# Performance work log

Hardware: AMD Instinct MI355X
Metric: run time of the kernel (lower is better)

## Reference

```python
import jax, jax.numpy as jnp
import numpy as np

# (C,H,W) of x0..x11; flattened size +1 homogeneous coordinate per key
SHAPES = [(3,32,32),(96,32,32),(96,32,32),(96,16,16),(192,16,16),(192,16,16),(192,8,8),(192,8,8),(192,8,8),(640,1,1),(100,1,1),(10,1,1)]
# (Cin,Cout,k,stride,pad) for conv1..conv9
CONV = [(3,96,3,1,1),(96,96,3,1,1),(96,96,3,2,1),(96,192,3,1,1),(192,192,3,1,1),(192,192,3,2,1),(192,192,3,1,1),(192,192,1,1,0),(192,10,1,1,0)]
B = 128


def setup_inputs():
    key = jax.random.key(0)
    inp = {}
    k, key = jax.random.split(key)
    inp['x0'] = jax.random.normal(k, (int(np.prod(SHAPES[0])) + 1, B), jnp.float32)
    for i, s in enumerate(SHAPES):
        n = int(np.prod(s)) + 1
        k1, k2, key = jax.random.split(key, 3)
        inp['perm%d' % i] = jax.random.permutation(k1, n)
        inp['diag%d' % i] = jax.random.uniform(k2, (n,), jnp.float32, 0.5, 1.5)
    for j, (ci, co, ks, st, pd) in enumerate(CONV):
        k1, k2, key = jax.random.split(key, 3)
        inp['w%d' % (j + 1)] = jax.random.normal(k1, (co, ci, ks, ks), jnp.float32) / np.float32(np.sqrt(ci * ks * ks))
        inp['b%d' % (j + 1)] = jax.random.normal(k2, (co,), jnp.float32) * 0.01
    k1, k2, k3, k4 = jax.random.split(key, 4)
    inp['fw1'] = jax.random.normal(k1, (100, 640), jnp.float32) / np.float32(np.sqrt(640))
    inp['fb1'] = jax.random.normal(k2, (100,), jnp.float32) * 0.01
    inp['fw2'] = jax.random.normal(k3, (10, 100), jnp.float32) / np.float32(np.sqrt(100))
    inp['fb2'] = jax.random.normal(k4, (10,), jnp.float32) * 0.01
    return inp


def _decode(x, perm, diag):
    # A_inv @ x with A_inv = P^T D^{-1}; P^T gather index is argsort(perm)
    return (x / diag[:, None])[jnp.argsort(perm)]


def _encode(y, perm, diag):
    # A @ y with A = D P; (P y)[i] = y[perm[i]]
    return diag[:, None] * y[perm]


def _conv_aug(v, w, b, shape_in, stride, pad):
    # affine-augmented conv: [W b; 0 1] applied to [feat; t]
    C, H, Wd = shape_in
    feat, t = v[:-1], v[-1]                      # (C*H*W, B), (B,)
    x = feat.T.reshape(-1, C, H, Wd)
    y = jax.lax.conv_general_dilated(x, w, (stride, stride), [(pad, pad), (pad, pad)],
                                     dimension_numbers=('NCHW', 'OIHW', 'NCHW'))
    y = y + b[None, :, None, None] * t[:, None, None, None]
    yf = y.reshape(y.shape[0], -1).T             # (N_out, B)
    return jnp.concatenate([yf, t[None, :]], axis=0)


def _fc_aug(v, w, b):
    feat, t = v[:-1], v[-1]
    return jnp.concatenate([w @ feat + b[:, None] * t[None, :], t[None, :]], axis=0)


def _forward(x0, perms, diags, ws, bs, fw1, fb1, fw2, fb2):
    x = x0
    for i in range(9):
        v = _decode(x, perms[i], diags[i])
        y = _conv_aug(v, ws[i], bs[i], SHAPES[i], CONV[i][3], CONV[i][4])
        x = jax.nn.relu(_encode(y, perms[i + 1], diags[i + 1]))
    v = _decode(x, perms[9], diags[9])
    x = jax.nn.relu(_encode(_fc_aug(v, fw1, fb1), perms[10], diags[10]))
    v = _decode(x, perms[10], diags[10])
    return _encode(_fc_aug(v, fw2, fb2), perms[11], diags[11])


def reference(x0, perm0, perm1, perm2, perm3, perm4, perm5, perm6, perm7, perm8, perm9, perm10, perm11,
              diag0, diag1, diag2, diag3, diag4, diag5, diag6, diag7, diag8, diag9, diag10, diag11,
              w1, b1, w2, b2, w3, b3, w4, b4, w5, b5, w6, b6, w7, b7, w8, b8, w9, b9,
              fw1, fb1, fw2, fb2):
    perms = [perm0, perm1, perm2, perm3, perm4, perm5, perm6, perm7, perm8, perm9, perm10, perm11]
    diags = [diag0, diag1, diag2, diag3, diag4, diag5, diag6, diag7, diag8, diag9, diag10, diag11]
    ws = [w1, w2, w3, w4, w5, w6, w7, w8, w9]
    bs = [b1, b2, b3, b4, b5, b6, b7, b8, b9]
    return _forward(x0, perms, diags, ws, bs, fw1, fb1, fw2, fb2)
```

## Files before the change

kernel.cpp:

```cpp
#include <hip/hip_runtime.h>


#define B 128
#define ZPAD 2048

typedef _Float16 f16_t;
typedef __attribute__((ext_vector_type(8))) _Float16 f16x8;
typedef __attribute__((ext_vector_type(4))) _Float16 f16x4;
typedef __attribute__((ext_vector_type(4))) float f32x4;


__global__ void decode_kernel(const float* __restrict__ x, const int* __restrict__ perm,
                              const float* __restrict__ diag, float* __restrict__ v, int nrows) {
    int row = blockIdx.x * 8 + (threadIdx.x >> 5);
    if (row >= nrows) return;
    int lane = threadIdx.x & 31;
    int p = perm[row];
    float inv = 1.0f / diag[row];
    float4 val = ((const float4*)(x + (size_t)row * B))[lane];
    val.x *= inv; val.y *= inv; val.z *= inv; val.w *= inv;
    ((float4*)(v + (size_t)p * B))[lane] = val;
}

__global__ void fc_kernel(const float* __restrict__ v, const float* __restrict__ w,
                          const float* __restrict__ b, float* __restrict__ y,
                          int K, int R, int do_relu) {
    int r = blockIdx.x;
    int n = threadIdx.x;
    float t = v[(size_t)K * B + n];
    float val;
    if (r == R) {
        val = t;
    } else {
        float a0 = 0.f, a1 = 0.f, a2 = 0.f, a3 = 0.f;
        float a4 = 0.f, a5 = 0.f, a6 = 0.f, a7 = 0.f;
        const float* wr = w + (size_t)r * K;
        int k = 0;
        for (; k + 8 <= K; k += 8) {
            float4 w0 = *(const float4*)(wr + k);
            float4 w1 = *(const float4*)(wr + k + 4);
            float x0 = v[(size_t)(k + 0) * B + n];
            float x1 = v[(size_t)(k + 1) * B + n];
            float x2 = v[(size_t)(k + 2) * B + n];
            float x3 = v[(size_t)(k + 3) * B + n];
            float x4 = v[(size_t)(k + 4) * B + n];
            float x5 = v[(size_t)(k + 5) * B + n];
            float x6 = v[(size_t)(k + 6) * B + n];
            float x7 = v[(size_t)(k + 7) * B + n];
            a0 = fmaf(w0.x, x0, a0);
            a1 = fmaf(w0.y, x1, a1);
            a2 = fmaf(w0.z, x2, a2);
            a3 = fmaf(w0.w, x3, a3);
            a4 = fmaf(w1.x, x4, a4);
            a5 = fmaf(w1.y, x5, a5);
            a6 = fmaf(w1.z, x6, a6);
            a7 = fmaf(w1.w, x7, a7);
        }
        for (; k < K; ++k)
            a0 = fmaf(wr[k], v[(size_t)k * B + n], a0);
        val = b[r] * t + ((a0 + a1) + (a2 + a3)) + ((a4 + a5) + (a6 + a7));
    }
    if (do_relu) val = fmaxf(val, 0.f);
    y[(size_t)r * B + n] = val;
}

__global__ void fc2_encode_kernel(const float* __restrict__ v, const float* __restrict__ w,
                                  const float* __restrict__ b, const int* __restrict__ perm,
                                  const float* __restrict__ diag, float* __restrict__ out) {
    int jrow = blockIdx.x;
    int n = threadIdx.x;
    int r = perm[jrow];
    float d = diag[jrow];
    float t = v[100 * B + n];
    float val;
    if (r == 10) {
        val = t;
    } else {
        float a0 = 0.f, a1 = 0.f, a2 = 0.f, a3 = 0.f;
        const float* wr = w + (size_t)r * 100;
        for (int k = 0; k < 100; k += 4) {
            float4 w4 = *(const float4*)(wr + k);
            a0 = fmaf(w4.x, v[(size_t)(k + 0) * B + n], a0);
            a1 = fmaf(w4.y, v[(size_t)(k + 1) * B + n], a1);
            a2 = fmaf(w4.z, v[(size_t)(k + 2) * B + n], a2);
            a3 = fmaf(w4.w, v[(size_t)(k + 3) * B + n], a3);
        }
        val = b[r] * t + (a0 + a1) + (a2 + a3);
    }
    out[(size_t)jrow * B + n] = d * val;
}


__global__ void pack_input_kernel(const float* __restrict__ v, f16_t* __restrict__ xout,
                                  float* __restrict__ tout) {
    int idx = blockIdx.x * 256 + threadIdx.x;
    int p = idx >> 7, n = idx & 127;
    f16x8 o = {};
    o[0] = (f16_t)v[(size_t)(0 * 1024 + p) * B + n];
    o[1] = (f16_t)v[(size_t)(1 * 1024 + p) * B + n];
    o[2] = (f16_t)v[(size_t)(2 * 1024 + p) * B + n];
    *(f16x8*)(xout + ZPAD + (size_t)p * 1024 + n * 8) = o;
    if (idx < B) tout[idx] = v[(size_t)3072 * B + idx];
}


struct WArgs {
    const float* w[9]; const float* b[9];
    int Ci[9], Co[9], KS[9], Cp[9], NCG[9];
    int woff[10]; int boff[10];
};

__global__ void pack_weights_kernel(WArgs A, f16_t* __restrict__ wp, float* __restrict__ bp,
                                    f16_t* __restrict__ x8a, f16_t* __restrict__ x8b) {
    int idx = blockIdx.x * 256 + threadIdx.x;
    if (idx < ZPAD) { x8a[idx] = (f16_t)0.f; x8b[idx] = (f16_t)0.f; }
    if (idx < A.boff[9]) {
        int l = 0;
        while (idx >= A.boff[l + 1]) ++l;
        int co = idx - A.boff[l];
        bp[idx] = (co < A.Co[l]) ? A.b[l][co] : 0.f;
    }
    if (idx >= A.woff[9]) return;
    int l = 0;
    while (idx >= A.woff[l + 1]) ++l;
    int e = idx - A.woff[l];
    int j = e & 7;
    int t1 = e >> 3;
    int Cp = A.Cp[l];
    int co = t1 % Cp;
    int gg = t1 / Cp;
    int ncg = A.NCG[l];
    int tap = gg / ncg, cg = gg - tap * ncg;
    int ks = A.KS[l];
    int kh = tap / ks, kw = tap - kh * ks;
    int ci = cg * 8 + j;
    float val = 0.f;
    if (co < A.Co[l] && tap < ks * ks && ci < A.Ci[l])
        val = A.w[l][(((size_t)co * A.Ci[l] + ci) * ks + kh) * ks + kw];
    wp[idx] = (f16_t)val;
}


template <int KS, int NS, int NSPLIT, int CBW, bool F32OUT>
__global__ __launch_bounds__(64 * CBW) void conv_mfma_kernel(
    const f16_t* __restrict__ xin, const float* __restrict__ t_in,
    const f16_t* __restrict__ wp, const float* __restrict__ bp,
    f16_t* __restrict__ xout, float* __restrict__ t_out, float* __restrict__ f32out,
    int Hi, int Wi, int Wo_log2, int HWo,
    int stride, int pad, int NCG, int nchunk, int KGr, int Co, int Co_pad,
    int PB8, int CB)
{
    constexpr int PF = 2;
    constexpr int MS = 4;
    const int wave = threadIdx.x >> 6;
    const int lane = threadIdx.x & 63;
    const int q = lane >> 4;
    const int r = lane & 15;

    const int gb = blockIdx.x;
    const int xcd = gb & 7;
    int j = gb >> 3;
    int nh = 0, cog, p;
    if (CBW > 1) {
        cog = wave;
        p = xcd * PB8 + j;
    } else {
        if (NSPLIT == 2) { nh = j & 1; j >>= 1; }
        cog = j % CB;
        p = xcd * PB8 + j / CB;
    }
    const int co0 = cog * 64;
    const int ncol0 = nh * (NS * 16);
    const int ncol8 = ncol0 * 8;

    const int ho = p >> Wo_log2;
    const int wo = p & ((1 << Wo_log2) - 1);
    const f16_t* xdata = xin + ZPAD;

    float tv[NS];
#pragma unroll
    for (int ns = 0; ns < NS; ++ns) tv[ns] = t_in[ncol0 + ns * 16 + r];

    f32x4 acc[MS][NS];
#pragma unroll
    for (int ms = 0; ms < MS; ++ms) {
        float4 b4 = *(const float4*)(bp + co0 + ms * 16 + q * 4);
#pragma unroll
        for (int ns = 0; ns < NS; ++ns) {
            acc[ms][ns][0] = b4.x * tv[ns];
            acc[ms][ns][1] = b4.y * tv[ns];
            acc[ms][ns][2] = b4.z * tv[ns];
            acc[ms][ns][3] = b4.w * tv[ns];
        }
    }

    const int hb = ho * stride - pad, wb = wo * stride - pad;
    const int HiWi = Hi * Wi;
    const int HiWi4 = 4 * HiWi;
    const int NCGHW = NCG * HiWi;
    const int wend = wb + KS;

    int g = q, cg = q, hi = hb, wi = wb, cgHW;
    {
        while (cg >= NCG) { cg -= NCG; ++wi; if (wi == wend) { wi = wb; ++hi; } }
        cgHW = cg * HiWi;
    }

    f16x8 bf[PF][NS], af[PF][MS];

    auto advance = [&]() {
        g += 4; cg += 4; cgHW += HiWi4;
        if (NCG >= 4) {
            int c2 = cg - NCG;
            bool wrap = c2 >= 0;
            int wn = wi + 1;
            bool ww = wrap & (wn == wend);
            cg   = wrap ? c2 : cg;
            cgHW = wrap ? cgHW - NCGHW : cgHW;
            wi   = wrap ? (ww ? wb : wn) : wi;
            hi   = ww ? hi + 1 : hi;
        } else {
            while (cg >= NCG) { cg -= NCG; cgHW -= NCGHW; ++wi; if (wi == wend) { wi = wb; ++hi; } }
        }
    };
    auto loadB = [&](f16x8* b) {
        bool v = (g < KGr) & ((unsigned)hi < (unsigned)Hi) & ((unsigned)wi < (unsigned)Wi);
        int boff = (cgHW + hi * Wi + wi) << 10;
        const f16_t* bb = xdata + (v ? boff : -ZPAD) + ncol8 + r * 8;
#pragma unroll
        for (int ns = 0; ns < NS; ++ns) b[ns] = *(const f16x8*)(bb + ns * 128);
    };
    auto loadA = [&](f16x8* a, int c) {
        int ac = c < nchunk ? c : nchunk - 1;
        const f16_t* ap = wp + (((ac * 4 + q) * Co_pad) + co0 + r) * 8;
#pragma unroll
        for (int ms = 0; ms < MS; ++ms) a[ms] = *(const f16x8*)(ap + ms * 128);
    };
    auto domfma = [&](f16x8* a, f16x8* b) {
#pragma unroll
        for (int ms = 0; ms < MS; ++ms)
#pragma unroll
            for (int ns = 0; ns < NS; ++ns)
                acc[ms][ns] = __builtin_amdgcn_mfma_f32_16x16x32_f16(a[ms], b[ns], acc[ms][ns], 0, 0, 0);
    };

#pragma unroll
    for (int pf = 0; pf < PF; ++pf) { loadB(bf[pf]); loadA(af[pf], pf); advance(); }
    const int nck = ((nchunk + PF - 1) / PF) * PF;
    for (int c = 0; c < nck; c += PF) {
#pragma unroll
        for (int pf = 0; pf < PF; ++pf) {
            domfma(af[pf], bf[pf]);
            loadB(bf[pf]); loadA(af[pf], c + PF + pf); advance();
        }
    }

    if (!F32OUT) {
#pragma unroll
        for (int ms = 0; ms < MS; ++ms) {
            int cob = co0 + ms * 16 + q * 4;
            if (cob < Co) {
                int off0 = ((cob >> 3) * HWo + p) * 1024 + (cob & 7) + ncol8 + r * 8;
#pragma unroll
                for (int ns = 0; ns < NS; ++ns) {
                    f16x4 h;
                    h[0] = (f16_t)fmaxf(acc[ms][ns][0], 0.f);
                    h[1] = (f16_t)fmaxf(acc[ms][ns][1], 0.f);
                    h[2] = (f16_t)fmaxf(acc[ms][ns][2], 0.f);
                    h[3] = (f16_t)fmaxf(acc[ms][ns][3], 0.f);
                    *(f16x4*)(xout + ZPAD + off0 + ns * 128) = h;
                }
            }
        }
        if (gb == 0) {
            for (int i = threadIdx.x; i < B; i += CBW * 64)
                t_out[i] = fmaxf(t_in[i], 0.f);
        }
    } else {
#pragma unroll
        for (int ms = 0; ms < MS; ++ms)
#pragma unroll
            for (int ns = 0; ns < NS; ++ns)
#pragma unroll
                for (int e = 0; e < 4; ++e) {
                    int co = co0 + ms * 16 + q * 4 + e;
                    if (co < Co)
                        f32out[((size_t)co * HWo + p) * B + ncol0 + ns * 16 + r] =
                            fmaxf(acc[ms][ns][e], 0.f);
                }
        if (gb == 0) {
            for (int i = threadIdx.x; i < B; i += CBW * 64)
                f32out[(size_t)Co * HWo * B + i] = fmaxf(t_in[i], 0.f);
        }
    }
}


extern "C" void kernel_launch(void* const* d_in, const int* in_sizes, int n_in,
                              void* d_out, int out_size, void* d_ws, size_t ws_size,
                              hipStream_t stream) {
    const float* x0 = (const float*)d_in[0];
    const int*   perm[12];
    const float* diag[12];
    for (int i = 0; i < 12; ++i) {
        perm[i] = (const int*)d_in[1 + 2 * i];
        diag[i] = (const float*)d_in[2 + 2 * i];
    }
    const float* wts[9];
    const float* bia[9];
    for (int j = 0; j < 9; ++j) {
        wts[j] = (const float*)d_in[25 + 2 * j];
        bia[j] = (const float*)d_in[26 + 2 * j];
    }
    const float* fw1 = (const float*)d_in[43];
    const float* fb1 = (const float*)d_in[44];
    const float* fw2 = (const float*)d_in[45];
    const float* fb2 = (const float*)d_in[46];
    float* out = (float*)d_out;

    static const int CiA[9]  = {3, 96, 96, 96, 192, 192, 192, 192, 192};
    static const int CoA[9]  = {96, 96, 96, 192, 192, 192, 192, 192, 10};
    static const int KSA[9]  = {3, 3, 3, 3, 3, 3, 3, 1, 1};
    static const int CpA[9]  = {128, 128, 128, 192, 192, 192, 192, 192, 64};
    static const int NCGA[9] = {1, 12, 12, 12, 24, 24, 24, 24, 24};
    static const int KGRA[9] = {9, 108, 108, 108, 216, 216, 216, 24, 24};
    static const int NCHK[9] = {3, 27, 27, 27, 54, 54, 54, 6, 6};
    static const int HiA[9]  = {32, 32, 32, 16, 16, 16, 8, 8, 8};
    static const int WoL[9]  = {5, 5, 4, 4, 4, 3, 3, 3, 3};
    static const int HWoA[9] = {1024, 1024, 256, 256, 256, 64, 64, 64, 64};
    static const int STA[9]  = {1, 1, 2, 1, 1, 2, 1, 1, 1};
    static const int PDA[9]  = {1, 1, 1, 1, 1, 1, 1, 0, 0};
    static const int NSPL[9] = {1, 1, 1, 1, 1, 2, 2, 2, 2};

    char* wsb = (char*)d_ws;
    const size_t BUF_F32  = 1574912;
    const size_t X8_BYTES = (size_t)(ZPAD + 12 * 1024 * 1024) * 2;
    float* bufA = (float*)wsb;
    float* bufB = (float*)(wsb + BUF_F32);
    f16_t* x8a  = (f16_t*)(wsb + 2 * BUF_F32);
    f16_t* x8b  = (f16_t*)(wsb + 2 * BUF_F32 + X8_BYTES);
    f16_t* wpb  = (f16_t*)(wsb + 2 * BUF_F32 + 2 * X8_BYTES);
    const size_t WP_BYTES = 2888704;
    float* bpb  = (float*)(wsb + 2 * BUF_F32 + 2 * X8_BYTES + WP_BYTES);
    float* t0   = (float*)((char*)bpb + 8192);
    float* t1   = t0 + 256;

    WArgs WA;
    int wo = 0, bo = 0;
    for (int l = 0; l < 9; ++l) {
        WA.w[l] = wts[l]; WA.b[l] = bia[l];
        WA.Ci[l] = CiA[l]; WA.Co[l] = CoA[l]; WA.KS[l] = KSA[l];
        WA.Cp[l] = CpA[l]; WA.NCG[l] = NCGA[l];
        WA.woff[l] = wo; wo += NCHK[l] * 4 * CpA[l] * 8;
        WA.boff[l] = bo; bo += CpA[l];
    }
    WA.woff[9] = wo; WA.boff[9] = bo;
    pack_weights_kernel<<<(wo + 255) / 256, 256, 0, stream>>>(WA, wpb, bpb, x8a, x8b);

    decode_kernel<<<(3073 + 7) / 8, 256, 0, stream>>>(x0, perm[0], diag[0], bufA, 3073);
    pack_input_kernel<<<131072 / 256, 256, 0, stream>>>(bufA, x8a, t0);

    f16_t* xin = x8a; f16_t* xout = x8b;
    float* tin = t0;  float* tout = t1;
    for (int l = 0; l < 9; ++l) {
        const int PB8 = HWoA[l] / 8;
        const int CB = CpA[l] / 64;
        const f16_t* wpl = wpb + WA.woff[l];
        const float* bpl = bpb + WA.boff[l];
        if (l <= 2) {
            conv_mfma_kernel<3, 8, 1, 2, false><<<8 * PB8, 128, 0, stream>>>(
                xin, tin, wpl, bpl, xout, tout, nullptr,
                HiA[l], HiA[l], WoL[l], HWoA[l], STA[l], PDA[l],
                NCGA[l], NCHK[l], KGRA[l], CoA[l], CpA[l], PB8, CB);
        } else if (l <= 4) {
            conv_mfma_kernel<3, 8, 1, 3, false><<<8 * PB8, 192, 0, stream>>>(
                xin, tin, wpl, bpl, xout, tout, nullptr,
                HiA[l], HiA[l], WoL[l], HWoA[l], STA[l], PDA[l],
                NCGA[l], NCHK[l], KGRA[l], CoA[l], CpA[l], PB8, CB);
        } else if (l <= 6) {
            conv_mfma_kernel<3, 4, 2, 1, false><<<8 * PB8 * CB * 2, 64, 0, stream>>>(
                xin, tin, wpl, bpl, xout, tout, nullptr,
                HiA[l], HiA[l], WoL[l], HWoA[l], STA[l], PDA[l],
                NCGA[l], NCHK[l], KGRA[l], CoA[l], CpA[l], PB8, CB);
        } else if (l == 7) {
            conv_mfma_kernel<1, 4, 2, 1, false><<<8 * PB8 * CB * 2, 64, 0, stream>>>(
                xin, tin, wpl, bpl, xout, tout, nullptr,
                HiA[l], HiA[l], WoL[l], HWoA[l], STA[l], PDA[l],
                NCGA[l], NCHK[l], KGRA[l], CoA[l], CpA[l], PB8, CB);
        } else {
            conv_mfma_kernel<1, 4, 2, 1, true><<<8 * PB8 * CB * 2, 64, 0, stream>>>(
                xin, tin, wpl, bpl, nullptr, nullptr, bufA,
                HiA[l], HiA[l], WoL[l], HWoA[l], STA[l], PDA[l],
                NCGA[l], NCHK[l], KGRA[l], CoA[l], CpA[l], PB8, CB);
        }
        f16_t* xt = xin; xin = xout; xout = xt;
        float* tt = tin; tin = tout; tout = tt;
    }

    fc_kernel<<<101, B, 0, stream>>>(bufA, fw1, fb1, bufB, 640, 100, 1);
    fc2_encode_kernel<<<11, B, 0, stream>>>(bufB, fw2, fb2, perm[11], diag[11], out);
}
```

Measured before the change: 330.3 us.

## Stage conv operand tiles through double-buffered LDS shared across waves

```diff
diff --git a/kernel.cpp b/kernel.cpp
--- a/kernel.cpp
+++ b/kernel.cpp
@@ -141,8 +141,193 @@
 }
 
 
-template <int KS, int NS, int NSPLIT, int CBW, bool F32OUT>
-__global__ __launch_bounds__(64 * CBW) void conv_mfma_kernel(
+template <int KS, int NS, int NSPLIT, int CBW, int CP, bool F32OUT>
+__global__ __launch_bounds__(64 * CBW, 2) void conv_lds_kernel(
+    const f16_t* __restrict__ xin, const float* __restrict__ t_in,
+    const f16_t* __restrict__ wp, const float* __restrict__ bp,
+    f16_t* __restrict__ xout, float* __restrict__ t_out, float* __restrict__ f32out,
+    int Hi, int Wi, int Wo_log2, int HWo,
+    int stride, int pad, int NCG, int nchunk, int KGr, int Co, int PB8)
+{
+    constexpr int MS = 4;
+    constexpr int ABYTES = CP * 64;
+    constexpr int BBYTES = NS * 1024;
+    constexpr int BUFSZ  = ABYTES + BBYTES;
+    constexpr int APIECE = CP / 16;
+    constexpr int BPIECE = NS;
+    constexpr int NPIECE = APIECE + BPIECE;
+    constexpr int NPT    = ((NPIECE + CBW - 1) / CBW) * CBW;
+    constexpr int S      = NPT / CBW;
+
+    __shared__ char smem[2 * BUFSZ];
+
+    const int wave = threadIdx.x >> 6;
+    const int lane = threadIdx.x & 63;
+    const int q = lane >> 4;
+    const int r = lane & 15;
+
+    const int gb = blockIdx.x;
+    const int xcd = gb & 7;
+    int j = gb >> 3;
+    int nh = 0;
+    if (NSPLIT == 2) { nh = j & 1; j >>= 1; }
+    const int p = xcd * PB8 + j;
+    const int co0 = wave * 64;
+    const int ncol0 = nh * (NS * 16);
+    const int ncol8 = ncol0 * 8;
+
+    const int ho = p >> Wo_log2;
+    const int wo = p & ((1 << Wo_log2) - 1);
+    const f16_t* xdata = xin + ZPAD;
+
+    float tv[NS];
+#pragma unroll
+    for (int ns = 0; ns < NS; ++ns) tv[ns] = t_in[ncol0 + ns * 16 + r];
+
+    f32x4 acc[MS][NS];
+#pragma unroll
+    for (int ms = 0; ms < MS; ++ms) {
+        float4 b4 = *(const float4*)(bp + co0 + ms * 16 + q * 4);
+#pragma unroll
+        for (int ns = 0; ns < NS; ++ns) {
+            acc[ms][ns][0] = b4.x * tv[ns];
+            acc[ms][ns][1] = b4.y * tv[ns];
+            acc[ms][ns][2] = b4.z * tv[ns];
+            acc[ms][ns][3] = b4.w * tv[ns];
+        }
+    }
+
+    const int hb = ho * stride - pad, wb = wo * stride - pad;
+    const int HiWi = Hi * Wi;
+    const int HiWi4 = 4 * HiWi;
+    const int NCGHW = NCG * HiWi;
+    const int wend = wb + KS;
+
+    int g4[4], cg4[4], hi4[4], wi4[4], cgHW4[4];
+#pragma unroll
+    for (int k = 0; k < 4; ++k) {
+        g4[k] = k; cg4[k] = k; hi4[k] = hb; wi4[k] = wb;
+        while (cg4[k] >= NCG) { cg4[k] -= NCG; ++wi4[k]; if (wi4[k] == wend) { wi4[k] = wb; ++hi4[k]; } }
+        cgHW4[k] = cg4[k] * HiWi;
+    }
+    auto advance = [&]() {
+#pragma unroll
+        for (int k = 0; k < 4; ++k) {
+            g4[k] += 4; cg4[k] += 4; cgHW4[k] += HiWi4;
+            while (cg4[k] >= NCG) { cg4[k] -= NCG; cgHW4[k] -= NCGHW; ++wi4[k]; if (wi4[k] == wend) { wi4[k] = wb; ++hi4[k]; } }
+        }
+    };
+
+    auto piece_loff = [&](int idx) {
+        int pi = (idx < NPIECE) ? idx : (idx - NPIECE + APIECE);
+        if (pi < APIECE) return pi * 1024;
+        int bi = pi - APIECE;
+        int k  = (NS == 8) ? (bi >> 1) : bi;
+        int jj = (NS == 8) ? (bi & 1) : 0;
+        return ABYTES + k * (NS * 256) + jj * 1024;
+    };
+
+    f16x8 sreg[S];
+    auto ldg = [&](int cc) {
+        const f16_t* abase = wp + (size_t)cc * 4 * CP * 8;
+        const f16_t* bslab[4];
+#pragma unroll
+        for (int k = 0; k < 4; ++k) {
+            bool v = (g4[k] < KGr) & ((unsigned)hi4[k] < (unsigned)Hi) & ((unsigned)wi4[k] < (unsigned)Wi);
+            int boff = (cgHW4[k] + hi4[k] * Wi + wi4[k]) << 10;
+            bslab[k] = xdata + (v ? boff : -ZPAD) + ncol8;
+        }
+#pragma unroll
+        for (int s = 0; s < S; ++s) {
+            int idx = wave + s * CBW;
+            int pi = (idx < NPIECE) ? idx : (idx - NPIECE + APIECE);
+            const f16_t* g;
+            if (pi < APIECE) {
+                g = abase + pi * 512;
+            } else {
+                int bi = pi - APIECE;
+                int k  = (NS == 8) ? (bi >> 1) : bi;
+                int jj = (NS == 8) ? (bi & 1) : 0;
+                g = bslab[k] + jj * 512;
+            }
+            sreg[s] = *(const f16x8*)(g + lane * 8);
+        }
+    };
+    auto dsw = [&](int cc) {
+        char* base = smem + (cc & 1) * BUFSZ;
+#pragma unroll
+        for (int s = 0; s < S; ++s) {
+            int loff = piece_loff(wave + s * CBW);
+            *(f16x8*)(base + loff + lane * 16) = sreg[s];
+        }
+    };
+    auto comp = [&](int cc) {
+        const char* base = smem + (cc & 1) * BUFSZ;
+        f16x8 af[MS], bf[NS];
+#pragma unroll
+        for (int ms = 0; ms < MS; ++ms)
+            af[ms] = *(const f16x8*)(base + ((q * CP) + co0 + ms * 16 + r) * 16);
+#pragma unroll
+        for (int ns = 0; ns < NS; ++ns)
+            bf[ns] = *(const f16x8*)(base + ABYTES + q * (NS * 256) + (ns * 16 + r) * 16);
+#pragma unroll
+        for (int ms = 0; ms < MS; ++ms)
+#pragma unroll
+            for (int ns = 0; ns < NS; ++ns)
+                acc[ms][ns] = __builtin_amdgcn_mfma_f32_16x16x32_f16(af[ms], bf[ns], acc[ms][ns], 0, 0, 0);
+    };
+
+    ldg(0); advance();
+    for (int c = 0; c < nchunk; ++c) {
+        dsw(c);
+        __syncthreads();
+        if (c + 1 < nchunk) { ldg(c + 1); advance(); }
+        comp(c);
+    }
+
+    if (!F32OUT) {
+#pragma unroll
+        for (int ms = 0; ms < MS; ++ms) {
+            int cob = co0 + ms * 16 + q * 4;
+            if (cob < Co) {
+                int off0 = ((cob >> 3) * HWo + p) * 1024 + (cob & 7) + ncol8 + r * 8;
+#pragma unroll
+                for (int ns = 0; ns < NS; ++ns) {
+                    f16x4 h;
+                    h[0] = (f16_t)fmaxf(acc[ms][ns][0], 0.f);
+                    h[1] = (f16_t)fmaxf(acc[ms][ns][1], 0.f);
+                    h[2] = (f16_t)fmaxf(acc[ms][ns][2], 0.f);
+                    h[3] = (f16_t)fmaxf(acc[ms][ns][3], 0.f);
+                    *(f16x4*)(xout + ZPAD + off0 + ns * 128) = h;
+                }
+            }
+        }
+        if (gb == 0) {
+            for (int i = threadIdx.x; i < B; i += 64 * CBW)
+                t_out[i] = fmaxf(t_in[i], 0.f);
+        }
+    } else {
+#pragma unroll
+        for (int ms = 0; ms < MS; ++ms)
+#pragma unroll
+            for (int ns = 0; ns < NS; ++ns)
+#pragma unroll
+                for (int e = 0; e < 4; ++e) {
+                    int co = co0 + ms * 16 + q * 4 + e;
+                    if (co < Co)
+                        f32out[((size_t)co * HWo + p) * B + ncol0 + ns * 16 + r] =
+                            fmaxf(acc[ms][ns][e], 0.f);
+                }
+        if (gb == 0) {
+            for (int i = threadIdx.x; i < B; i += 64 * CBW)
+                f32out[(size_t)Co * HWo * B + i] = fmaxf(t_in[i], 0.f);
+        }
+    }
+}
+
+
+template <int KS, int NS, int NSPLIT, bool F32OUT>
+__global__ __launch_bounds__(64) void conv_mfma_kernel(
     const f16_t* __restrict__ xin, const float* __restrict__ t_in,
     const f16_t* __restrict__ wp, const float* __restrict__ bp,
     f16_t* __restrict__ xout, float* __restrict__ t_out, float* __restrict__ f32out,
@@ -152,7 +337,6 @@
 {
     constexpr int PF = 2;
     constexpr int MS = 4;
-    const int wave = threadIdx.x >> 6;
     const int lane = threadIdx.x & 63;
     const int q = lane >> 4;
     const int r = lane & 15;
@@ -160,15 +344,10 @@
     const int gb = blockIdx.x;
     const int xcd = gb & 7;
     int j = gb >> 3;
-    int nh = 0, cog, p;
-    if (CBW > 1) {
-        cog = wave;
-        p = xcd * PB8 + j;
-    } else {
-        if (NSPLIT == 2) { nh = j & 1; j >>= 1; }
-        cog = j % CB;
-        p = xcd * PB8 + j / CB;
-    }
+    int nh = 0;
+    if (NSPLIT == 2) { nh = j & 1; j >>= 1; }
+    const int cog = j % CB;
+    const int p = xcd * PB8 + j / CB;
     const int co0 = cog * 64;
     const int ncol0 = nh * (NS * 16);
     const int ncol8 = ncol0 * 8;
@@ -273,7 +452,7 @@
             }
         }
         if (gb == 0) {
-            for (int i = threadIdx.x; i < B; i += CBW * 64)
+            for (int i = threadIdx.x; i < B; i += 64)
                 t_out[i] = fmaxf(t_in[i], 0.f);
         }
     } else {
@@ -289,7 +468,7 @@
                             fmaxf(acc[ms][ns][e], 0.f);
                 }
         if (gb == 0) {
-            for (int i = threadIdx.x; i < B; i += CBW * 64)
+            for (int i = threadIdx.x; i < B; i += 64)
                 f32out[(size_t)Co * HWo * B + i] = fmaxf(t_in[i], 0.f);
         }
     }
@@ -330,7 +509,6 @@
     static const int HWoA[9] = {1024, 1024, 256, 256, 256, 64, 64, 64, 64};
     static const int STA[9]  = {1, 1, 2, 1, 1, 2, 1, 1, 1};
     static const int PDA[9]  = {1, 1, 1, 1, 1, 1, 1, 0, 0};
-    static const int NSPL[9] = {1, 1, 1, 1, 1, 2, 2, 2, 2};
 
     char* wsb = (char*)d_ws;
     const size_t BUF_F32  = 1574912;
@@ -367,28 +545,33 @@
         const int CB = CpA[l] / 64;
         const f16_t* wpl = wpb + WA.woff[l];
         const float* bpl = bpb + WA.boff[l];
-        if (l <= 2) {
-            conv_mfma_kernel<3, 8, 1, 2, false><<<8 * PB8, 128, 0, stream>>>(
+        if (l <= 1) {
+            conv_lds_kernel<3, 8, 1, 2, 128, false><<<8 * PB8, 128, 0, stream>>>(
                 xin, tin, wpl, bpl, xout, tout, nullptr,
                 HiA[l], HiA[l], WoL[l], HWoA[l], STA[l], PDA[l],
-                NCGA[l], NCHK[l], KGRA[l], CoA[l], CpA[l], PB8, CB);
-        } else if (l <= 4) {
-            conv_mfma_kernel<3, 8, 1, 3, false><<<8 * PB8, 192, 0, stream>>>(
+                NCGA[l], NCHK[l], KGRA[l], CoA[l], PB8);
+        } else if (l == 2) {
+            conv_lds_kernel<3, 4, 2, 2, 128, false><<<8 * PB8 * 2, 128, 0, stream>>>(
                 xin, tin, wpl, bpl, xout, tout, nullptr,
                 HiA[l], HiA[l], WoL[l], HWoA[l], STA[l], PDA[l],
-                NCGA[l], NCHK[l], KGRA[l], CoA[l], CpA[l], PB8, CB);
+                NCGA[l], NCHK[l], KGRA[l], CoA[l], PB8);
+        } else if (l <= 4) {
+            conv_lds_kernel<3, 4, 2, 3, 192, false><<<8 * PB8 * 2, 192, 0, stream>>>(
+                xin, tin, wpl, bpl, xout, tout, nullptr,
+                HiA[l], HiA[l], WoL[l], HWoA[l], STA[l], PDA[l],
+                NCGA[l], NCHK[l], KGRA[l], CoA[l], PB8);
         } else if (l <= 6) {
-            conv_mfma_kernel<3, 4, 2, 1, false><<<8 * PB8 * CB * 2, 64, 0, stream>>>(
+            conv_mfma_kernel<3, 4, 2, false><<<8 * PB8 * CB * 2, 64, 0, stream>>>(
                 xin, tin, wpl, bpl, xout, tout, nullptr,
                 HiA[l], HiA[l], WoL[l], HWoA[l], STA[l], PDA[l],
                 NCGA[l], NCHK[l], KGRA[l], CoA[l], CpA[l], PB8, CB);
         } else if (l == 7) {
-            conv_mfma_kernel<1, 4, 2, 1, false><<<8 * PB8 * CB * 2, 64, 0, stream>>>(
+            conv_mfma_kernel<1, 4, 2, false><<<8 * PB8 * CB * 2, 64, 0, stream>>>(
                 xin, tin, wpl, bpl, xout, tout, nullptr,
                 HiA[l], HiA[l], WoL[l], HWoA[l], STA[l], PDA[l],
                 NCGA[l], NCHK[l], KGRA[l], CoA[l], CpA[l], PB8, CB);
         } else {
-            conv_mfma_kernel<1, 4, 2, 1, true><<<8 * PB8 * CB * 2, 64, 0, stream>>>(
+            conv_mfma_kernel<1, 4, 2, true><<<8 * PB8 * CB * 2, 64, 0, stream>>>(
                 xin, tin, wpl, bpl, nullptr, nullptr, bufA,
                 HiA[l], HiA[l], WoL[l], HWoA[l], STA[l], PDA[l],
                 NCGA[l], NCHK[l], KGRA[l], CoA[l], CpA[l], PB8, CB);
```

After: 407.4 us. 1.23x slower.

## Add LDS double-buffered async-copy conv kernel for layers 1, 3 and 4

Applied to the files above, without the earlier changes.

```diff
diff --git a/kernel.cpp b/kernel.cpp
--- a/kernel.cpp
+++ b/kernel.cpp
@@ -8,6 +8,13 @@
 typedef __attribute__((ext_vector_type(8))) _Float16 f16x8;
 typedef __attribute__((ext_vector_type(4))) _Float16 f16x4;
 typedef __attribute__((ext_vector_type(4))) float f32x4;
+
+__device__ __forceinline__ void async_copy16(const f16_t* g, char* l) {
+    __builtin_amdgcn_global_load_lds(
+        (const __attribute__((address_space(1))) void*)g,
+        (__attribute__((address_space(3))) void*)l,
+        16, 0, 0);
+}
 
 
 __global__ void decode_kernel(const float* __restrict__ x, const int* __restrict__ perm,
@@ -141,6 +148,168 @@
 }
 
 
+template <int NS, int NSPLIT, int PX, int COG, int CP>
+__global__ __launch_bounds__(64 * PX * COG, (PX * COG == 4) ? 2 : 3)
+void conv_async_kernel(
+    const f16_t* __restrict__ xin, const float* __restrict__ t_in,
+    const f16_t* __restrict__ wp, const float* __restrict__ bp,
+    f16_t* __restrict__ xout, float* __restrict__ t_out,
+    int Hi, int Wi, int Wo_log2, int HWo, int stride, int pad,
+    int NCG, int nchunk, int KGr, int Co, int PPB8)
+{
+    constexpr int W = PX * COG;
+    constexpr int AP = CP / 16;
+    constexpr int NSP = NS / 4;
+    constexpr int BP = PX * 4 * NSP;
+    constexpr int NP = AP + BP;
+    constexpr int ABYTES = CP * 64;
+    constexpr int BUFSZ = ABYTES + BP * 1024;
+    constexpr int MS = 4;
+
+    __shared__ char smem[2 * BUFSZ];
+
+    const int wave = threadIdx.x >> 6;
+    const int lane = threadIdx.x & 63;
+    const int q = lane >> 4;
+    const int r = lane & 15;
+    const int px_me = wave / COG;
+    const int cg_me = wave - px_me * COG;
+    const int co0 = cg_me * 64;
+
+    const int gb = blockIdx.x;
+    const int xcd = gb & 7;
+    int j = gb >> 3;
+    int nh = 0;
+    if (NSPLIT == 2) { nh = j & 1; j >>= 1; }
+    const int pp = xcd * PPB8 + j;
+    const int ncol0 = nh * (NS * 16);
+    const int ncol8 = ncol0 * 8;
+
+    const f16_t* xdata = xin + ZPAD;
+    const int HiWi = Hi * Wi;
+
+    int hbb[PX], wbb[PX];
+#pragma unroll
+    for (int px = 0; px < PX; ++px) {
+        int p_ = pp * PX + px;
+        int ho = p_ >> Wo_log2, wo = p_ & ((1 << Wo_log2) - 1);
+        hbb[px] = ho * stride - pad;
+        wbb[px] = wo * stride - pad;
+    }
+    const int p_me = pp * PX + px_me;
+
+    float tv[NS];
+#pragma unroll
+    for (int ns = 0; ns < NS; ++ns) tv[ns] = t_in[ncol0 + ns * 16 + r];
+
+    f32x4 acc[MS][NS];
+#pragma unroll
+    for (int ms = 0; ms < MS; ++ms) {
+        float4 b4 = *(const float4*)(bp + co0 + ms * 16 + q * 4);
+#pragma unroll
+        for (int ns = 0; ns < NS; ++ns) {
+            acc[ms][ns][0] = b4.x * tv[ns];
+            acc[ms][ns][1] = b4.y * tv[ns];
+            acc[ms][ns][2] = b4.z * tv[ns];
+            acc[ms][ns][3] = b4.w * tv[ns];
+        }
+    }
+
+    int g4[4], cg4[4], kh4[4], kw4[4];
+#pragma unroll
+    for (int k = 0; k < 4; ++k) { g4[k] = k; cg4[k] = k; kh4[k] = 0; kw4[k] = 0; }
+
+    auto stage = [&](int cc) {
+        const f16_t* abase = wp + (size_t)cc * (4 * CP * 8);
+        const f16_t* slab[PX][4];
+#pragma unroll
+        for (int k = 0; k < 4; ++k) {
+            bool gv = (g4[k] < KGr);
+            int khk = kh4[k], kwk = kw4[k];
+            int cgHW = cg4[k] * HiWi;
+#pragma unroll
+            for (int px = 0; px < PX; ++px) {
+                int hi = hbb[px] + khk, wi = wbb[px] + kwk;
+                bool v = gv & ((unsigned)hi < (unsigned)Hi) & ((unsigned)wi < (unsigned)Wi);
+                int boff = (cgHW + hi * Wi + wi) << 10;
+                slab[px][k] = xdata + (v ? boff : -ZPAD) + ncol8;
+            }
+        }
+        char* base = smem + (cc & 1) * BUFSZ;
+#pragma unroll
+        for (int idx = wave; idx < NP; idx += W) {
+            const f16_t* g;
+            int loff;
+            if (idx < AP) {
+                g = abase + idx * 512;
+                loff = idx * 1024;
+            } else {
+                int bi = idx - AP;
+                int sub = (NSP == 2) ? (bi & 1) : 0;
+                int pk  = (NSP == 2) ? (bi >> 1) : bi;
+                int px = pk >> 2, k = pk & 3;
+                g = slab[px][k] + sub * 512;
+                loff = ABYTES + bi * 1024;
+            }
+            async_copy16(g + lane * 8, base + loff);
+        }
+#pragma unroll
+        for (int k = 0; k < 4; ++k) {
+            g4[k] += 4; cg4[k] += 4;
+            if (cg4[k] >= NCG) {
+                cg4[k] -= NCG;
+                ++kw4[k];
+                if (kw4[k] == 3) { kw4[k] = 0; ++kh4[k]; }
+            }
+        }
+    };
+
+    auto comp = [&](int cc) {
+        const char* base = smem + (cc & 1) * BUFSZ;
+        f16x8 af[MS], bf[NS];
+#pragma unroll
+        for (int ms = 0; ms < MS; ++ms)
+            af[ms] = *(const f16x8*)(base + (q * CP + co0 + ms * 16 + r) * 16);
+#pragma unroll
+        for (int ns = 0; ns < NS; ++ns)
+            bf[ns] = *(const f16x8*)(base + ABYTES + (px_me * 4 + q) * (NSP * 1024) + (ns * 16 + r) * 16);
+#pragma unroll
+        for (int ms = 0; ms < MS; ++ms)
+#pragma unroll
+            for (int ns = 0; ns < NS; ++ns)
+                acc[ms][ns] = __builtin_amdgcn_mfma_f32_16x16x32_f16(af[ms], bf[ns], acc[ms][ns], 0, 0, 0);
+    };
+
+    stage(0);
+    for (int c = 0; c < nchunk; ++c) {
+        __syncthreads();
+        if (c + 1 < nchunk) stage(c + 1);
+        comp(c);
+    }
+
+#pragma unroll
+    for (int ms = 0; ms < MS; ++ms) {
+        int cob = co0 + ms * 16 + q * 4;
+        if (cob < Co) {
+            int off0 = ((cob >> 3) * HWo + p_me) * 1024 + (cob & 7) + ncol8 + r * 8;
+#pragma unroll
+            for (int ns = 0; ns < NS; ++ns) {
+                f16x4 h;
+                h[0] = (f16_t)fmaxf(acc[ms][ns][0], 0.f);
+                h[1] = (f16_t)fmaxf(acc[ms][ns][1], 0.f);
+                h[2] = (f16_t)fmaxf(acc[ms][ns][2], 0.f);
+                h[3] = (f16_t)fmaxf(acc[ms][ns][3], 0.f);
+                *(f16x4*)(xout + ZPAD + off0 + ns * 128) = h;
+            }
+        }
+    }
+    if (gb == 0) {
+        for (int i = threadIdx.x; i < B; i += 64 * W)
+            t_out[i] = fmaxf(t_in[i], 0.f);
+    }
+}
+
+
 template <int KS, int NS, int NSPLIT, int CBW, bool F32OUT>
 __global__ __launch_bounds__(64 * CBW) void conv_mfma_kernel(
     const f16_t* __restrict__ xin, const float* __restrict__ t_in,
@@ -273,7 +442,7 @@
             }
         }
         if (gb == 0) {
-            for (int i = threadIdx.x; i < B; i += CBW * 64)
+            for (int i = threadIdx.x; i < B; i += 64 * CBW)
                 t_out[i] = fmaxf(t_in[i], 0.f);
         }
     } else {
@@ -289,7 +458,7 @@
                             fmaxf(acc[ms][ns][e], 0.f);
                 }
         if (gb == 0) {
-            for (int i = threadIdx.x; i < B; i += CBW * 64)
+            for (int i = threadIdx.x; i < B; i += 64 * CBW)
                 f32out[(size_t)Co * HWo * B + i] = fmaxf(t_in[i], 0.f);
         }
     }
@@ -330,7 +499,6 @@
     static const int HWoA[9] = {1024, 1024, 256, 256, 256, 64, 64, 64, 64};
     static const int STA[9]  = {1, 1, 2, 1, 1, 2, 1, 1, 1};
     static const int PDA[9]  = {1, 1, 1, 1, 1, 1, 1, 0, 0};
-    static const int NSPL[9] = {1, 1, 1, 1, 1, 2, 2, 2, 2};
 
     char* wsb = (char*)d_ws;
     const size_t BUF_F32  = 1574912;
@@ -367,16 +535,26 @@
         const int CB = CpA[l] / 64;
         const f16_t* wpl = wpb + WA.woff[l];
         const float* bpl = bpb + WA.boff[l];
-        if (l <= 2) {
+        if (l == 0) {
             conv_mfma_kernel<3, 8, 1, 2, false><<<8 * PB8, 128, 0, stream>>>(
                 xin, tin, wpl, bpl, xout, tout, nullptr,
                 HiA[l], HiA[l], WoL[l], HWoA[l], STA[l], PDA[l],
                 NCGA[l], NCHK[l], KGRA[l], CoA[l], CpA[l], PB8, CB);
+        } else if (l == 1) {
+            conv_async_kernel<8, 1, 2, 2, 128><<<8 * (HWoA[l] / 16), 256, 0, stream>>>(
+                xin, tin, wpl, bpl, xout, tout,
+                HiA[l], HiA[l], WoL[l], HWoA[l], STA[l], PDA[l],
+                NCGA[l], NCHK[l], KGRA[l], CoA[l], HWoA[l] / 16);
+        } else if (l == 2) {
+            conv_mfma_kernel<3, 8, 1, 2, false><<<8 * PB8, 128, 0, stream>>>(
+                xin, tin, wpl, bpl, xout, tout, nullptr,
+                HiA[l], HiA[l], WoL[l], HWoA[l], STA[l], PDA[l],
+                NCGA[l], NCHK[l], KGRA[l], CoA[l], CpA[l], PB8, CB);
         } else if (l <= 4) {
-            conv_mfma_kernel<3, 8, 1, 3, false><<<8 * PB8, 192, 0, stream>>>(
-                xin, tin, wpl, bpl, xout, tout, nullptr,
-                HiA[l], HiA[l], WoL[l], HWoA[l], STA[l], PDA[l],
-                NCGA[l], NCHK[l], KGRA[l], CoA[l], CpA[l], PB8, CB);
+            conv_async_kernel<4, 2, 2, 3, 192><<<8 * (HWoA[l] / 16) * 2, 384, 0, stream>>>(
+                xin, tin, wpl, bpl, xout, tout,
+                HiA[l], HiA[l], WoL[l], HWoA[l], STA[l], PDA[l],
+                NCGA[l], NCHK[l], KGRA[l], CoA[l], HWoA[l] / 16);
         } else if (l <= 6) {
             conv_mfma_kernel<3, 4, 2, 1, false><<<8 * PB8 * CB * 2, 64, 0, stream>>>(
                 xin, tin, wpl, bpl, xout, tout, nullptr,
```

Result: slower. 499.8 us (+51.3%).

## Fuse input decode with f16 packing and split batch columns across more blocks

Applied to the files above, without the earlier changes.

```diff
diff --git a/kernel.cpp b/kernel.cpp
--- a/kernel.cpp
+++ b/kernel.cpp
@@ -10,17 +10,22 @@
 typedef __attribute__((ext_vector_type(4))) float f32x4;
 
 
-__global__ void decode_kernel(const float* __restrict__ x, const int* __restrict__ perm,
-                              const float* __restrict__ diag, float* __restrict__ v, int nrows) {
-    int row = blockIdx.x * 8 + (threadIdx.x >> 5);
-    if (row >= nrows) return;
-    int lane = threadIdx.x & 31;
-    int p = perm[row];
-    float inv = 1.0f / diag[row];
-    float4 val = ((const float4*)(x + (size_t)row * B))[lane];
-    val.x *= inv; val.y *= inv; val.z *= inv; val.w *= inv;
-    ((float4*)(v + (size_t)p * B))[lane] = val;
-}
+__global__ void decode_pack_kernel(const float* __restrict__ x, const int* __restrict__ perm,
+                                   const float* __restrict__ diag,
+                                   f16_t* __restrict__ xout, float* __restrict__ tout) {
+    int row = blockIdx.x * 2 + (threadIdx.x >> 7);
+    if (row >= 3073) return;
+    int n = threadIdx.x & 127;
+    int i = perm[row];
+    float val = x[(size_t)row * B + n] / diag[row];
+    if (i < 3072) {
+        int c = i >> 10, p = i & 1023;
+        xout[ZPAD + p * 1024 + n * 8 + c] = (f16_t)val;
+    } else {
+        tout[n] = val;
+    }
+}
+
 
 __global__ void fc_kernel(const float* __restrict__ v, const float* __restrict__ w,
                           const float* __restrict__ b, float* __restrict__ y,
@@ -91,19 +96,6 @@
 }
 
 
-__global__ void pack_input_kernel(const float* __restrict__ v, f16_t* __restrict__ xout,
-                                  float* __restrict__ tout) {
-    int idx = blockIdx.x * 256 + threadIdx.x;
-    int p = idx >> 7, n = idx & 127;
-    f16x8 o = {};
-    o[0] = (f16_t)v[(size_t)(0 * 1024 + p) * B + n];
-    o[1] = (f16_t)v[(size_t)(1 * 1024 + p) * B + n];
-    o[2] = (f16_t)v[(size_t)(2 * 1024 + p) * B + n];
-    *(f16x8*)(xout + ZPAD + (size_t)p * 1024 + n * 8) = o;
-    if (idx < B) tout[idx] = v[(size_t)3072 * B + idx];
-}
-
-
 struct WArgs {
     const float* w[9]; const float* b[9];
     int Ci[9], Co[9], KS[9], Cp[9], NCG[9];
@@ -113,7 +105,8 @@
 __global__ void pack_weights_kernel(WArgs A, f16_t* __restrict__ wp, float* __restrict__ bp,
                                     f16_t* __restrict__ x8a, f16_t* __restrict__ x8b) {
     int idx = blockIdx.x * 256 + threadIdx.x;
-    if (idx < ZPAD) { x8a[idx] = (f16_t)0.f; x8b[idx] = (f16_t)0.f; }
+    if (idx < ZPAD + 1048576) x8a[idx] = (f16_t)0.f;
+    if (idx < ZPAD) x8b[idx] = (f16_t)0.f;
     if (idx < A.boff[9]) {
         int l = 0;
         while (idx >= A.boff[l + 1]) ++l;
@@ -161,11 +154,11 @@
     const int xcd = gb & 7;
     int j = gb >> 3;
     int nh = 0, cog, p;
+    if (NSPLIT > 1) { nh = j % NSPLIT; j /= NSPLIT; }
     if (CBW > 1) {
         cog = wave;
         p = xcd * PB8 + j;
     } else {
-        if (NSPLIT == 2) { nh = j & 1; j >>= 1; }
         cog = j % CB;
         p = xcd * PB8 + j / CB;
     }
@@ -273,7 +266,7 @@
             }
         }
         if (gb == 0) {
-            for (int i = threadIdx.x; i < B; i += CBW * 64)
+            for (int i = threadIdx.x; i < B; i += 64 * CBW)
                 t_out[i] = fmaxf(t_in[i], 0.f);
         }
     } else {
@@ -289,7 +282,7 @@
                             fmaxf(acc[ms][ns][e], 0.f);
                 }
         if (gb == 0) {
-            for (int i = threadIdx.x; i < B; i += CBW * 64)
+            for (int i = threadIdx.x; i < B; i += 64 * CBW)
                 f32out[(size_t)Co * HWo * B + i] = fmaxf(t_in[i], 0.f);
         }
     }
@@ -330,7 +323,6 @@
     static const int HWoA[9] = {1024, 1024, 256, 256, 256, 64, 64, 64, 64};
     static const int STA[9]  = {1, 1, 2, 1, 1, 2, 1, 1, 1};
     static const int PDA[9]  = {1, 1, 1, 1, 1, 1, 1, 0, 0};
-    static const int NSPL[9] = {1, 1, 1, 1, 1, 2, 2, 2, 2};
 
     char* wsb = (char*)d_ws;
     const size_t BUF_F32  = 1574912;
@@ -357,8 +349,7 @@
     WA.woff[9] = wo; WA.boff[9] = bo;
     pack_weights_kernel<<<(wo + 255) / 256, 256, 0, stream>>>(WA, wpb, bpb, x8a, x8b);
 
-    decode_kernel<<<(3073 + 7) / 8, 256, 0, stream>>>(x0, perm[0], diag[0], bufA, 3073);
-    pack_input_kernel<<<131072 / 256, 256, 0, stream>>>(bufA, x8a, t0);
+    decode_pack_kernel<<<(3073 + 1) / 2, 256, 0, stream>>>(x0, perm[0], diag[0], x8a, t0);
 
     f16_t* xin = x8a; f16_t* xout = x8b;
     float* tin = t0;  float* tout = t1;
@@ -367,8 +358,13 @@
         const int CB = CpA[l] / 64;
         const f16_t* wpl = wpb + WA.woff[l];
         const float* bpl = bpb + WA.boff[l];
-        if (l <= 2) {
+        if (l <= 1) {
             conv_mfma_kernel<3, 8, 1, 2, false><<<8 * PB8, 128, 0, stream>>>(
+                xin, tin, wpl, bpl, xout, tout, nullptr,
+                HiA[l], HiA[l], WoL[l], HWoA[l], STA[l], PDA[l],
+                NCGA[l], NCHK[l], KGRA[l], CoA[l], CpA[l], PB8, CB);
+        } else if (l == 2) {
+            conv_mfma_kernel<3, 4, 2, 2, false><<<8 * PB8 * 2, 128, 0, stream>>>(
                 xin, tin, wpl, bpl, xout, tout, nullptr,
                 HiA[l], HiA[l], WoL[l], HWoA[l], STA[l], PDA[l],
                 NCGA[l], NCHK[l], KGRA[l], CoA[l], CpA[l], PB8, CB);
@@ -378,17 +374,17 @@
                 HiA[l], HiA[l], WoL[l], HWoA[l], STA[l], PDA[l],
                 NCGA[l], NCHK[l], KGRA[l], CoA[l], CpA[l], PB8, CB);
         } else if (l <= 6) {
-            conv_mfma_kernel<3, 4, 2, 1, false><<<8 * PB8 * CB * 2, 64, 0, stream>>>(
+            conv_mfma_kernel<3, 2, 4, 1, false><<<8 * PB8 * CB * 4, 64, 0, stream>>>(
                 xin, tin, wpl, bpl, xout, tout, nullptr,
                 HiA[l], HiA[l], WoL[l], HWoA[l], STA[l], PDA[l],
                 NCGA[l], NCHK[l], KGRA[l], CoA[l], CpA[l], PB8, CB);
         } else if (l == 7) {
-            conv_mfma_kernel<1, 4, 2, 1, false><<<8 * PB8 * CB * 2, 64, 0, stream>>>(
+            conv_mfma_kernel<1, 2, 4, 1, false><<<8 * PB8 * CB * 4, 64, 0, stream>>>(
                 xin, tin, wpl, bpl, xout, tout, nullptr,
                 HiA[l], HiA[l], WoL[l], HWoA[l], STA[l], PDA[l],
                 NCGA[l], NCHK[l], KGRA[l], CoA[l], CpA[l], PB8, CB);
         } else {
-            conv_mfma_kernel<1, 4, 2, 1, true><<<8 * PB8 * CB * 2, 64, 0, stream>>>(
+            conv_mfma_kernel<1, 2, 4, 1, true><<<8 * PB8 * CB * 4, 64, 0, stream>>>(
                 xin, tin, wpl, bpl, nullptr, nullptr, bufA,
                 HiA[l], HiA[l], WoL[l], HWoA[l], STA[l], PDA[l],
                 NCGA[l], NCHK[l], KGRA[l], CoA[l], CpA[l], PB8, CB);
```

Result: faster. 321.7 us (-2.6%).
